# Optimization experiments

Hardware: AMD Instinct MI355X
Metric: run time of the kernel (lower is better)

Reference implementation:

```python
import jax, jax.numpy as jnp
import numpy as np

B, S, H = 8, 1024, 768      # batch, seq_len, encoder hidden
T, D = 9, 64                # output_type_size, att_dim
NEG = -1e12                 # masked_fill value from original code


def rope_tables(seq_len, dim):
    # theta_i = 10000^(-2i/dim), repeat_interleave(2) -> [t0,t0,t1,t1,...]
    pos = jnp.arange(seq_len, dtype=jnp.float32)[:, None]           # [S,1]
    theta = jnp.power(10000.0, -2.0 * jnp.arange(dim // 2, dtype=jnp.float32) / dim)
    theta = jnp.repeat(theta, 2)                                     # [D]
    ang = pos * theta[None, :]                                       # [S,D]
    return jnp.cos(ang), jnp.sin(ang)


def setup_inputs() -> dict:
    key = jax.random.key(0)
    k1, k2 = jax.random.split(key)
    hidden = jax.random.normal(k1, (B, S, H), dtype=jnp.float32)
    attention_mask = jnp.ones((B, S), dtype=jnp.int32)
    # xavier_normal-ish init for dense weight [2*T*D, H], zero bias
    fan = H + T * D * 2
    W = jax.random.normal(k2, (T * D * 2, H), dtype=jnp.float32) * (2.0 / fan) ** 0.5
    b = jnp.zeros((T * D * 2,), dtype=jnp.float32)
    return {"hidden": hidden, "attention_mask": attention_mask, "W": W, "b": b}


def reference(hidden, attention_mask, W, b):
    Bsz, Sl, _ = hidden.shape
    out = hidden @ W.T + b                          # [B,S,2*T*D]
    out = out.reshape(Bsz, Sl, T, D, 2)
    q = out[..., 0].transpose(0, 2, 1, 3)           # [B,T,S,D]
    k = out[..., 1].transpose(0, 2, 1, 3)           # [B,T,S,D]

    cos, sin = rope_tables(Sl, D)                   # [S,D] each

    def rot(x):
        # faithful to original: cat([-x[...,1::2], x[...,::2]], -1), NOT interleaved
        x2 = jnp.concatenate([-x[..., 1::2], x[..., ::2]], axis=-1)
        return x * cos + x2 * sin

    q, k = rot(q), rot(k)

    logits = jnp.einsum('btmd,btnd->btmn', q, k)    # [B,T,S,S]

    am = attention_mask.astype(bool)
    pad = am[:, None, :, None] & am[:, None, None, :]   # [B,1,S,S]
    triu = jnp.triu(jnp.ones((Sl, Sl), dtype=bool))     # spans i<=j
    return jnp.where(pad & triu, logits, NEG)
```

## Files before the change

### kernel.cpp

```cpp
#include <hip/hip_runtime.h>

#define S_LEN 1024
#define HID   768
#define T_SZ  9
#define NEG_VAL (-1e12f)

typedef __bf16 bf16x8 __attribute__((ext_vector_type(8)));
typedef float  f32x4  __attribute__((ext_vector_type(4)));
typedef short  short8 __attribute__((ext_vector_type(8)));
typedef short  short4v __attribute__((ext_vector_type(4)));
typedef float  float4v __attribute__((ext_vector_type(4)));

__device__ __forceinline__ unsigned short f2bf(float f) {
    unsigned int u = __builtin_bit_cast(unsigned int, f);
    u += 0x7FFFu + ((u >> 16) & 1u);
    return (unsigned short)(u >> 16);
}

__global__ void k_tables(float* __restrict__ cosT, float* __restrict__ sinT) {
    int idx = blockIdx.x * 256 + threadIdx.x;
    int s = idx >> 6;
    int d = idx & 63;
    float theta = powf(10000.0f, -2.0f * (float)(d >> 1) * (1.0f / 64.0f));
    float ang = (float)s * theta;
    float sv, cv;
    sincosf(ang, &sv, &cv);
    cosT[idx] = cv;
    sinT[idx] = sv;
}

__global__ __launch_bounds__(256) void k_proj_rope(
    const float* __restrict__ hidden,
    const float* __restrict__ W,
    const float* __restrict__ bias,
    const float* __restrict__ cosT,
    const float* __restrict__ sinT,
    unsigned short* __restrict__ qout,
    unsigned short* __restrict__ kout)
{
    __shared__ union {
        struct { unsigned short A[128 * 64]; unsigned short B[128 * 64]; } st;
        unsigned short Tr[128 * 136];
    } sm;

    int tid = threadIdx.x;
    int mt = blockIdx.x / 9;
    int t  = blockIdx.x % 9;
    int m0 = mt * 128;
    int n0 = t * 128;

    int lane = tid & 63;
    int wave = tid >> 6;
    int lr = lane & 15;
    int lq = lane >> 4;
    int wrow = wave * 32;

    float bv[8];
    #pragma unroll
    for (int fn = 0; fn < 8; ++fn) bv[fn] = bias[n0 + fn * 16 + lr];

    int srow = tid >> 1;
    int half = tid & 1;
    const float* aSrc = hidden + (size_t)(m0 + srow) * HID + half * 32;
    const float* bSrc = W      + (size_t)(n0 + srow) * HID + half * 32;

    f32x4 acc[2][8];
    #pragma unroll
    for (int i = 0; i < 2; ++i)
        #pragma unroll
        for (int j = 0; j < 8; ++j) acc[i][j] = (f32x4){0.f, 0.f, 0.f, 0.f};

    for (int kk = 0; kk < HID / 64; ++kk) {
        __syncthreads();
        #pragma unroll
        for (int which = 0; which < 2; ++which) {
            const float* src = which ? bSrc : aSrc;
            unsigned short* dst = which ? sm.st.B : sm.st.A;
            #pragma unroll
            for (int sgi = 0; sgi < 4; ++sgi) {
                float4v v0 = *(const float4v*)(src + kk * 64 + sgi * 8);
                float4v v1 = *(const float4v*)(src + kk * 64 + sgi * 8 + 4);
                short8 p;
                p[0] = (short)f2bf(v0[0]); p[1] = (short)f2bf(v0[1]);
                p[2] = (short)f2bf(v0[2]); p[3] = (short)f2bf(v0[3]);
                p[4] = (short)f2bf(v1[0]); p[5] = (short)f2bf(v1[1]);
                p[6] = (short)f2bf(v1[2]); p[7] = (short)f2bf(v1[3]);
                int seg = half * 4 + sgi;
                *(short8*)&dst[srow * 64 + ((seg ^ (srow & 7)) * 8)] = p;
            }
        }
        __syncthreads();
        #pragma unroll
        for (int kb = 0; kb < 2; ++kb) {
            bf16x8 af[2];
            #pragma unroll
            for (int fm = 0; fm < 2; ++fm) {
                int r = wrow + fm * 16 + lr;
                int seg = kb * 4 + lq;
                af[fm] = *(const bf16x8*)&sm.st.A[r * 64 + ((seg ^ (r & 7)) * 8)];
            }
            #pragma unroll
            for (int fn = 0; fn < 8; ++fn) {
                int r = fn * 16 + lr;
                int seg = kb * 4 + lq;
                bf16x8 bfr = *(const bf16x8*)&sm.st.B[r * 64 + ((seg ^ (r & 7)) * 8)];
                acc[0][fn] = __builtin_amdgcn_mfma_f32_16x16x32_bf16(af[0], bfr, acc[0][fn], 0, 0, 0);
                acc[1][fn] = __builtin_amdgcn_mfma_f32_16x16x32_bf16(af[1], bfr, acc[1][fn], 0, 0, 0);
            }
        }
    }
    __syncthreads();

    #pragma unroll
    for (int fm = 0; fm < 2; ++fm) {
        #pragma unroll
        for (int fn = 0; fn < 8; ++fn) {
            int col = fn * 16 + lr;
            int r0 = wrow + fm * 16 + lq * 4;
            short4v pk;
            #pragma unroll
            for (int j = 0; j < 4; ++j) pk[j] = (short)f2bf(acc[fm][fn][j] + bv[fn]);
            *(short4v*)&sm.Tr[col * 136 + r0] = pk;
        }
    }
    __syncthreads();

    int d = tid & 63;
    int grp = tid >> 6;
    int cq = 2 * d, ck = 2 * d + 1;
    int pq = (d < 32) ? (4 * d + 2) : (4 * (d - 32));
    int pk2 = pq + 1;
    float sgn = (d < 32) ? -1.0f : 1.0f;
    #pragma unroll
    for (int ch = 0; ch < 4; ++ch) {
        int r0 = grp * 32 + ch * 8;
        bf16x8 xq = *(const bf16x8*)&sm.Tr[cq * 136 + r0];
        bf16x8 xk = *(const bf16x8*)&sm.Tr[ck * 136 + r0];
        bf16x8 yq = *(const bf16x8*)&sm.Tr[pq * 136 + r0];
        bf16x8 yk = *(const bf16x8*)&sm.Tr[pk2 * 136 + r0];
        #pragma unroll
        for (int rr = 0; rr < 8; ++rr) {
            int gm = m0 + r0 + rr;
            int s  = gm & (S_LEN - 1);
            int bb = gm >> 10;
            float cv = cosT[s * 64 + d];
            float sv = sinT[s * 64 + d];
            float qv = (float)xq[rr] * cv + sgn * (float)yq[rr] * sv;
            float kv = (float)xk[rr] * cv + sgn * (float)yk[rr] * sv;
            size_t ob = (((size_t)bb * T_SZ + t) * S_LEN + s) * 64 + d;
            qout[ob] = f2bf(qv);
            kout[ob] = f2bf(kv);
        }
    }
}

__global__ __launch_bounds__(256) void k_logits(
    const unsigned short* __restrict__ q,
    const unsigned short* __restrict__ k,
    const int* __restrict__ mask,
    float* __restrict__ out)
{
    int tid = threadIdx.x;
    int bt  = blockIdx.x >> 6;
    int rem = blockIdx.x & 63;
    int ti = rem >> 3;
    int tj = rem & 7;
    size_t obase = ((size_t)bt * S_LEN + (size_t)ti * 128) * S_LEN + tj * 128;

    if (ti > tj) {
        float4v nv = {NEG_VAL, NEG_VAL, NEG_VAL, NEG_VAL};
        #pragma unroll
        for (int it = 0; it < 16; ++it) {
            int idx = it * 256 + tid;
            int r = idx >> 5;
            int c4 = idx & 31;
            *(float4v*)&out[obase + (size_t)r * S_LEN + c4 * 4] = nv;
        }
        return;
    }

    __shared__ unsigned short As[128 * 64];
    __shared__ unsigned short Bs[128 * 64];
    __shared__ int mi[128], mj[128];

    int b = bt / 9;
    if (tid < 128) mi[tid] = mask[b * S_LEN + ti * 128 + tid];
    else           mj[tid - 128] = mask[b * S_LEN + tj * 128 + (tid - 128)];

    const unsigned short* qsrc = q + ((size_t)bt * S_LEN + (size_t)ti * 128) * 64;
    const unsigned short* ksrc = k + ((size_t)bt * S_LEN + (size_t)tj * 128) * 64;
    #pragma unroll
    for (int it = 0; it < 4; ++it) {
        int r = it * 32 + (tid >> 3);
        int seg = tid & 7;
        short8 vq = *(const short8*)&qsrc[r * 64 + seg * 8];
        short8 vk = *(const short8*)&ksrc[r * 64 + seg * 8];
        int sw = (seg ^ (r & 7)) * 8;
        *(short8*)&As[r * 64 + sw] = vq;
        *(short8*)&Bs[r * 64 + sw] = vk;
    }
    __syncthreads();

    int lane = tid & 63;
    int wave = tid >> 6;
    int lr = lane & 15;
    int lq = lane >> 4;
    int wrow = wave * 32;

    f32x4 acc[2][8];
    #pragma unroll
    for (int i = 0; i < 2; ++i)
        #pragma unroll
        for (int j = 0; j < 8; ++j) acc[i][j] = (f32x4){0.f, 0.f, 0.f, 0.f};

    #pragma unroll
    for (int kb = 0; kb < 2; ++kb) {
        bf16x8 af[2];
        #pragma unroll
        for (int fm = 0; fm < 2; ++fm) {
            int r = wrow + fm * 16 + lr;
            int seg = kb * 4 + lq;
            af[fm] = *(const bf16x8*)&As[r * 64 + ((seg ^ (r & 7)) * 8)];
        }
        #pragma unroll
        for (int fn = 0; fn < 8; ++fn) {
            int r = fn * 16 + lr;
            int seg = kb * 4 + lq;
            bf16x8 bfr = *(const bf16x8*)&Bs[r * 64 + ((seg ^ (r & 7)) * 8)];
            acc[0][fn] = __builtin_amdgcn_mfma_f32_16x16x32_bf16(af[0], bfr, acc[0][fn], 0, 0, 0);
            acc[1][fn] = __builtin_amdgcn_mfma_f32_16x16x32_bf16(af[1], bfr, acc[1][fn], 0, 0, 0);
        }
    }

    #pragma unroll
    for (int fm = 0; fm < 2; ++fm) {
        #pragma unroll
        for (int j = 0; j < 4; ++j) {
            int il = wrow + fm * 16 + lq * 4 + j;
            int gi = ti * 128 + il;
            int mrow = mi[il];
            size_t rbase = obase + (size_t)il * S_LEN;
            #pragma unroll
            for (int fn = 0; fn < 8; ++fn) {
                int jl = fn * 16 + lr;
                int gj = tj * 128 + jl;
                bool ok = (gi <= gj) && mrow && mj[jl];
                out[rbase + jl] = ok ? acc[fm][fn][j] : NEG_VAL;
            }
        }
    }
}

extern "C" void kernel_launch(void* const* d_in, const int* in_sizes, int n_in,
                              void* d_out, int out_size, void* d_ws, size_t ws_size,
                              hipStream_t stream) {
    const float* hidden = (const float*)d_in[0];
    const int*   mask   = (const int*)d_in[1];
    const float* W      = (const float*)d_in[2];
    const float* bias   = (const float*)d_in[3];
    float* out = (float*)d_out;
    int Bsz = in_sizes[0] / (S_LEN * HID);

    char* ws = (char*)d_ws;
    float* cosT = (float*)ws;
    float* sinT = (float*)(ws + (size_t)S_LEN * 64 * 4);
    unsigned short* qb = (unsigned short*)(ws + 2ull * S_LEN * 64 * 4);
    size_t qkElems = (size_t)Bsz * T_SZ * S_LEN * 64;
    unsigned short* kb = qb + qkElems;

    k_tables<<<dim3(S_LEN * 64 / 256), dim3(256), 0, stream>>>(cosT, sinT);
    k_proj_rope<<<dim3(Bsz * 8 * 9), dim3(256), 0, stream>>>(hidden, W, bias, cosT, sinT, qb, kb);
    k_logits<<<dim3(Bsz * T_SZ * 64), dim3(256), 0, stream>>>(qb, kb, mask, out);
}
```

Baseline: 410.1 us.

## Pre-convert inputs to bf16 and use direct global-to-LDS loads with vectorized stores

Adds a separate conversion pass that casts hidden and W to bf16 once, so the projection GEMM no longer re-reads fp32 data and converts it in every tile. Both the projection and the logits kernels now stage their tiles with global_load_lds into swizzled LDS. The logits MFMA operands are swapped so each lane holds four consecutive columns, allowing 16-byte nontemporal stores of the large output. This costs extra launches and a round trip of the bf16 copies through memory, and the rope table now uses exp2f instead of powf.

Measured after the change: 378.6 us. -7.7%, faster.

```diff
diff --git a/kernel.cpp b/kernel.cpp
--- a/kernel.cpp
+++ b/kernel.cpp
@@ -17,11 +17,33 @@
     return (unsigned short)(u >> 16);
 }
 
+__device__ __forceinline__ void gload_lds16(const void* g, void* l) {
+    __builtin_amdgcn_global_load_lds(
+        (const __attribute__((address_space(1))) unsigned int*)g,
+        (__attribute__((address_space(3))) unsigned int*)l,
+        16, 0, 0);
+}
+
+__global__ __launch_bounds__(256) void k_convert(const float* __restrict__ src,
+                                                 unsigned short* __restrict__ dst,
+                                                 int n8) {
+    int i = blockIdx.x * 256 + threadIdx.x;
+    if (i >= n8) return;
+    float4v a = *((const float4v*)src + (size_t)i * 2);
+    float4v b = *((const float4v*)src + (size_t)i * 2 + 1);
+    short8 o;
+    o[0] = (short)f2bf(a[0]); o[1] = (short)f2bf(a[1]);
+    o[2] = (short)f2bf(a[2]); o[3] = (short)f2bf(a[3]);
+    o[4] = (short)f2bf(b[0]); o[5] = (short)f2bf(b[1]);
+    o[6] = (short)f2bf(b[2]); o[7] = (short)f2bf(b[3]);
+    *(short8*)(dst + (size_t)i * 8) = o;
+}
+
 __global__ void k_tables(float* __restrict__ cosT, float* __restrict__ sinT) {
     int idx = blockIdx.x * 256 + threadIdx.x;
     int s = idx >> 6;
     int d = idx & 63;
-    float theta = powf(10000.0f, -2.0f * (float)(d >> 1) * (1.0f / 64.0f));
+    float theta = exp2f(-13.2877123795f * (float)(d >> 1) * (1.0f / 32.0f));
     float ang = (float)s * theta;
     float sv, cv;
     sincosf(ang, &sv, &cv);
@@ -30,15 +52,15 @@
 }
 
 __global__ __launch_bounds__(256) void k_proj_rope(
-    const float* __restrict__ hidden,
-    const float* __restrict__ W,
+    const unsigned short* __restrict__ hidB,
+    const unsigned short* __restrict__ wB,
     const float* __restrict__ bias,
     const float* __restrict__ cosT,
     const float* __restrict__ sinT,
     unsigned short* __restrict__ qout,
     unsigned short* __restrict__ kout)
 {
-    __shared__ union {
+    __shared__ union __align__(16) {
         struct { unsigned short A[128 * 64]; unsigned short B[128 * 64]; } st;
         unsigned short Tr[128 * 136];
     } sm;
@@ -59,10 +81,17 @@
     #pragma unroll
     for (int fn = 0; fn < 8; ++fn) bv[fn] = bias[n0 + fn * 16 + lr];
 
-    int srow = tid >> 1;
-    int half = tid & 1;
-    const float* aSrc = hidden + (size_t)(m0 + srow) * HID + half * 32;
-    const float* bSrc = W      + (size_t)(n0 + srow) * HID + half * 32;
+    const unsigned short* aSrc[4];
+    const unsigned short* bSrc[4];
+    #pragma unroll
+    for (int it = 0; it < 4; ++it) {
+        int gsi = (wave * 4 + it) * 64 + lane;
+        int r = gsi >> 3;
+        int sw = gsi & 7;
+        int seg8 = (sw ^ (r & 7)) << 3;
+        aSrc[it] = hidB + (size_t)(m0 + r) * HID + seg8;
+        bSrc[it] = wB  + (size_t)(n0 + r) * HID + seg8;
+    }
 
     f32x4 acc[2][8];
     #pragma unroll
@@ -73,21 +102,9 @@
     for (int kk = 0; kk < HID / 64; ++kk) {
         __syncthreads();
         #pragma unroll
-        for (int which = 0; which < 2; ++which) {
-            const float* src = which ? bSrc : aSrc;
-            unsigned short* dst = which ? sm.st.B : sm.st.A;
-            #pragma unroll
-            for (int sgi = 0; sgi < 4; ++sgi) {
-                float4v v0 = *(const float4v*)(src + kk * 64 + sgi * 8);
-                float4v v1 = *(const float4v*)(src + kk * 64 + sgi * 8 + 4);
-                short8 p;
-                p[0] = (short)f2bf(v0[0]); p[1] = (short)f2bf(v0[1]);
-                p[2] = (short)f2bf(v0[2]); p[3] = (short)f2bf(v0[3]);
-                p[4] = (short)f2bf(v1[0]); p[5] = (short)f2bf(v1[1]);
-                p[6] = (short)f2bf(v1[2]); p[7] = (short)f2bf(v1[3]);
-                int seg = half * 4 + sgi;
-                *(short8*)&dst[srow * 64 + ((seg ^ (srow & 7)) * 8)] = p;
-            }
+        for (int it = 0; it < 4; ++it) {
+            gload_lds16(aSrc[it] + kk * 64, &sm.st.A[(wave * 4 + it) * 512]);
+            gload_lds16(bSrc[it] + kk * 64, &sm.st.B[(wave * 4 + it) * 512]);
         }
         __syncthreads();
         #pragma unroll
@@ -174,13 +191,13 @@
             int idx = it * 256 + tid;
             int r = idx >> 5;
             int c4 = idx & 31;
-            *(float4v*)&out[obase + (size_t)r * S_LEN + c4 * 4] = nv;
+            __builtin_nontemporal_store(nv, (float4v*)&out[obase + (size_t)r * S_LEN + c4 * 4]);
         }
         return;
     }
 
-    __shared__ unsigned short As[128 * 64];
-    __shared__ unsigned short Bs[128 * 64];
+    __shared__ __align__(16) unsigned short As[128 * 64];
+    __shared__ __align__(16) unsigned short Bs[128 * 64];
     __shared__ int mi[128], mj[128];
 
     int b = bt / 9;
@@ -189,20 +206,20 @@
 
     const unsigned short* qsrc = q + ((size_t)bt * S_LEN + (size_t)ti * 128) * 64;
     const unsigned short* ksrc = k + ((size_t)bt * S_LEN + (size_t)tj * 128) * 64;
-    #pragma unroll
-    for (int it = 0; it < 4; ++it) {
-        int r = it * 32 + (tid >> 3);
-        int seg = tid & 7;
-        short8 vq = *(const short8*)&qsrc[r * 64 + seg * 8];
-        short8 vk = *(const short8*)&ksrc[r * 64 + seg * 8];
-        int sw = (seg ^ (r & 7)) * 8;
-        *(short8*)&As[r * 64 + sw] = vq;
-        *(short8*)&Bs[r * 64 + sw] = vk;
-    }
-    __syncthreads();
 
     int lane = tid & 63;
     int wave = tid >> 6;
+    #pragma unroll
+    for (int it = 0; it < 4; ++it) {
+        int gsi = (wave * 4 + it) * 64 + lane;
+        int r = gsi >> 3;
+        int sw = gsi & 7;
+        int off = r * 64 + ((sw ^ (r & 7)) << 3);
+        gload_lds16(qsrc + off, &As[(wave * 4 + it) * 512]);
+        gload_lds16(ksrc + off, &Bs[(wave * 4 + it) * 512]);
+    }
+    __syncthreads();
+
     int lr = lane & 15;
     int lq = lane >> 4;
     int wrow = wave * 32;
@@ -215,38 +232,40 @@
 
     #pragma unroll
     for (int kb = 0; kb < 2; ++kb) {
-        bf16x8 af[2];
-        #pragma unroll
-        for (int fm = 0; fm < 2; ++fm) {
-            int r = wrow + fm * 16 + lr;
+        bf16x8 qf[2];
+        #pragma unroll
+        for (int fi = 0; fi < 2; ++fi) {
+            int r = wrow + fi * 16 + lr;
             int seg = kb * 4 + lq;
-            af[fm] = *(const bf16x8*)&As[r * 64 + ((seg ^ (r & 7)) * 8)];
+            qf[fi] = *(const bf16x8*)&As[r * 64 + ((seg ^ (r & 7)) * 8)];
         }
         #pragma unroll
         for (int fn = 0; fn < 8; ++fn) {
             int r = fn * 16 + lr;
             int seg = kb * 4 + lq;
-            bf16x8 bfr = *(const bf16x8*)&Bs[r * 64 + ((seg ^ (r & 7)) * 8)];
-            acc[0][fn] = __builtin_amdgcn_mfma_f32_16x16x32_bf16(af[0], bfr, acc[0][fn], 0, 0, 0);
-            acc[1][fn] = __builtin_amdgcn_mfma_f32_16x16x32_bf16(af[1], bfr, acc[1][fn], 0, 0, 0);
-        }
-    }
-
-    #pragma unroll
-    for (int fm = 0; fm < 2; ++fm) {
-        #pragma unroll
-        for (int j = 0; j < 4; ++j) {
-            int il = wrow + fm * 16 + lq * 4 + j;
-            int gi = ti * 128 + il;
-            int mrow = mi[il];
-            size_t rbase = obase + (size_t)il * S_LEN;
+            bf16x8 kf = *(const bf16x8*)&Bs[r * 64 + ((seg ^ (r & 7)) * 8)];
+            acc[0][fn] = __builtin_amdgcn_mfma_f32_16x16x32_bf16(kf, qf[0], acc[0][fn], 0, 0, 0);
+            acc[1][fn] = __builtin_amdgcn_mfma_f32_16x16x32_bf16(kf, qf[1], acc[1][fn], 0, 0, 0);
+        }
+    }
+
+    #pragma unroll
+    for (int fi = 0; fi < 2; ++fi) {
+        int il = wrow + fi * 16 + lr;
+        int gi = ti * 128 + il;
+        bool mrow = mi[il] != 0;
+        size_t rbase = obase + (size_t)il * S_LEN;
+        #pragma unroll
+        for (int fn = 0; fn < 8; ++fn) {
+            int j0 = fn * 16 + lq * 4;
+            int gj0 = tj * 128 + j0;
+            float4v v;
             #pragma unroll
-            for (int fn = 0; fn < 8; ++fn) {
-                int jl = fn * 16 + lr;
-                int gj = tj * 128 + jl;
-                bool ok = (gi <= gj) && mrow && mj[jl];
-                out[rbase + jl] = ok ? acc[fm][fn][j] : NEG_VAL;
+            for (int e = 0; e < 4; ++e) {
+                bool ok = mrow && (mj[j0 + e] != 0) && (gi <= gj0 + e);
+                v[e] = ok ? acc[fi][fn][e] : NEG_VAL;
             }
+            __builtin_nontemporal_store(v, (float4v*)&out[rbase + j0]);
         }
     }
 }
@@ -264,11 +283,19 @@
     char* ws = (char*)d_ws;
     float* cosT = (float*)ws;
     float* sinT = (float*)(ws + (size_t)S_LEN * 64 * 4);
-    unsigned short* qb = (unsigned short*)(ws + 2ull * S_LEN * 64 * 4);
+    unsigned short* hidB = (unsigned short*)(ws + 2ull * S_LEN * 64 * 4);
+    size_t hidElems = (size_t)Bsz * S_LEN * HID;
+    unsigned short* wB = hidB + hidElems;
+    size_t wElems = (size_t)2 * T_SZ * 64 * HID;
+    unsigned short* qb = wB + wElems;
     size_t qkElems = (size_t)Bsz * T_SZ * S_LEN * 64;
     unsigned short* kb = qb + qkElems;
 
+    int n8h = (int)(hidElems / 8);
+    int n8w = (int)(wElems / 8);
+    k_convert<<<dim3((n8h + 255) / 256), dim3(256), 0, stream>>>(hidden, hidB, n8h);
+    k_convert<<<dim3((n8w + 255) / 256), dim3(256), 0, stream>>>(W, wB, n8w);
     k_tables<<<dim3(S_LEN * 64 / 256), dim3(256), 0, stream>>>(cosT, sinT);
-    k_proj_rope<<<dim3(Bsz * 8 * 9), dim3(256), 0, stream>>>(hidden, W, bias, cosT, sinT, qb, kb);
+    k_proj_rope<<<dim3(Bsz * 8 * 9), dim3(256), 0, stream>>>(hidB, wB, bias, cosT, sinT, qb, kb);
     k_logits<<<dim3(Bsz * T_SZ * 64), dim3(256), 0, stream>>>(qb, kb, mask, out);
 }
```
